# Performance work log

Measured on AMD Instinct MI355X. Metric: run time of the kernel, lower is better.

## Reference

```python
import jax, jax.numpy as jnp
import numpy as np

DIM = 100      # eqn.dim
NDIS = 50      # net_config['Ndis']
DT = 0.02      # net_config['dt']
LAM = 1.0      # HJB driver coefficient
HID = 110      # int_layers width
B = 8192       # batch


def setup_inputs() -> dict:
    key = jax.random.key(0)
    ks = jax.random.split(key, 6)
    dw = jax.random.normal(ks[0], (B, DIM, NDIS), jnp.float32) * np.float32(np.sqrt(DT))
    x = jax.random.normal(ks[1], (B, DIM, NDIS), jnp.float32)
    # z_net: Linear(dim+1 -> 110, no bias), ReLU, Linear(110 -> 110), ReLU, Linear(110 -> dim)
    W1 = (jax.random.normal(ks[2], (DIM + 1, HID), jnp.float32) / np.float32(np.sqrt(DIM + 1)))
    W2 = (jax.random.normal(ks[3], (HID, HID), jnp.float32) / np.float32(np.sqrt(HID)))
    W3 = (jax.random.normal(ks[4], (HID, DIM), jnp.float32) / np.float32(np.sqrt(HID)))
    y0 = jax.random.uniform(ks[5], (1,), jnp.float32)  # in_region=False scalar parameter
    return {"dw": dw, "x": x, "W1": W1, "W2": W2, "W3": W3, "y0": y0}


def reference(dw, x, W1, W2, W3, y0):
    # dw, x: [B, DIM, NDIS]
    ts = jnp.arange(NDIS, dtype=jnp.float32) * DT          # time_stamp
    xs = jnp.transpose(x, (2, 0, 1))                        # [T, B, DIM]
    dws = jnp.transpose(dw, (2, 0, 1))                      # [T, B, DIM]
    y_init = jnp.ones((dw.shape[0], 1), jnp.float32) * y0   # all_one_vec * y_0

    def step(y, inputs):
        t, xt, dwt = inputs
        # inp = hstack([t * all_one_vec, x[:, :, t]])  -> [B, DIM+1]
        inp = jnp.concatenate([jnp.ones((xt.shape[0], 1), xt.dtype) * t, xt], axis=1)
        h = jax.nn.relu(inp @ W1)
        h = jax.nn.relu(h @ W2)
        z = (h @ W3) / DIM                                   # [B, DIM]
        f = -LAM * jnp.sum(z * z, axis=1, keepdims=True)     # HJB driver f_tf
        y = y - DT * f + jnp.sum(z * dwt, axis=1, keepdims=True)
        return y, None

    y, _ = jax.lax.scan(step, y_init, (ts, xs, dws))
    return y  # [B, 1]
```

## Files before the change

kernel.cpp:

```cpp
#include <hip/hip_runtime.h>
#include <hip/hip_fp16.h>


#define DIMX 100
#define TS   50
#define TPAD 64
#define HID  110
#define K1   101
#define KA   120
#define NB   2
#define MROWS 128
#define DTCO 0.02f

typedef _Float16 f16;
typedef _Float16 f16x8 __attribute__((ext_vector_type(8)));
typedef float    f32x16 __attribute__((ext_vector_type(16)));

#define W1ROW 0
#define W3ROW 110
#define W2ROW 210
#define WROWS 338

__device__ __forceinline__ void mlp_layer(const f16* __restrict__ A,
                                          const f16* __restrict__ Wt,
                                          int m, int nh, int ln, int hi,
                                          f32x16& acc0, f32x16& acc1)
{
    const int arow = m * 32 + ln;
#pragma unroll
    for (int ks = 0; ks < 7; ++ks) {
        const f16x8 a   = *(const f16x8*)(A  + arow * KA            + ks * 16 + hi * 8);
        const f16x8 bv0 = *(const f16x8*)(Wt + (64 * nh      + ln) * KA + ks * 16 + hi * 8);
        const f16x8 bv1 = *(const f16x8*)(Wt + (64 * nh + 32 + ln) * KA + ks * 16 + hi * 8);
        acc0 = __builtin_amdgcn_mfma_f32_32x32x16_f16(a, bv0, acc0, 0, 0, 0);
        acc1 = __builtin_amdgcn_mfma_f32_32x32x16_f16(a, bv1, acc1, 0, 0, 0);
    }
}

__device__ __forceinline__ void store_h(f16* __restrict__ H, const f32x16& acc0,
                                        const f32x16& acc1, int m, int nh, int ln, int hi)
{
#pragma unroll
    for (int j = 0; j < 2; ++j) {
        const int col = 64 * nh + 32 * j + ln;
        if (col < HID) {
#pragma unroll
            for (int q = 0; q < 16; ++q) {
                const int row = 32 * m + (q & 3) + 8 * (q >> 2) + 4 * hi;
                float v = j ? acc1[q] : acc0[q];
                v = v > 0.f ? v : 0.f;
                H[row * KA + col] = (f16)v;
            }
        } else if (col < 112) {
#pragma unroll
            for (int q = 0; q < 16; ++q) {
                const int row = 32 * m + (q & 3) + 8 * (q >> 2) + 4 * hi;
                H[row * KA + col] = (f16)0.f;
            }
        }
    }
}

__launch_bounds__(512, 2)
__global__ void bsde_kernel(const float* __restrict__ dw, const float* __restrict__ x,
                            const float* __restrict__ W1, const float* __restrict__ W2,
                            const float* __restrict__ W3, const float* __restrict__ y0,
                            float* __restrict__ out)
{
    __shared__ __align__(16) f16 wlds[WROWS * KA];
    __shared__ __align__(16) f16 buf0[MROWS * KA];
    __shared__ __align__(16) f16 buf1[MROWS * KA];
    __shared__ float yacc[MROWS];

    const int tid  = threadIdx.x;
    const int lane = tid & 63;
    const int w    = tid >> 6;
    const int ln   = lane & 31;
    const int hi   = lane >> 5;
    const int m    = w >> 1;
    const int nh   = w & 1;

    for (int i = tid; i < WROWS * KA; i += 512) wlds[i] = (f16)0.f;
    __syncthreads();
    for (int e = tid; e < K1 * HID; e += 512) {
        const int k = e / HID, n = e % HID;
        wlds[(W1ROW + n) * KA + k] = (f16)W1[e];
    }
    for (int e = tid; e < HID * HID; e += 512) {
        const int k = e / HID, n = e % HID;
        wlds[(W2ROW + n) * KA + k] = (f16)W2[e];
    }
    for (int e = tid; e < HID * DIMX; e += 512) {
        const int k = e / DIMX, n = e % DIMX;
        wlds[(W3ROW + n) * KA + k] = (f16)W3[e];
    }
    for (int i = tid; i < MROWS * 11; i += 512) {
        const int r = i / 11, c = 101 + i % 11;
        buf0[r * KA + c] = (f16)0.f;
    }
    __syncthreads();

    const int   b0base = blockIdx.x * 32;
    const float yinit  = y0[0];

    for (int g = 0; g < 16; ++g) {
        const int b0 = b0base + 2 * g;

        if (tid < MROWS) yacc[tid] = 0.f;
        if (tid >= MROWS && tid < 2 * MROWS) {
            const int r = tid - MROWS, t = r & 63;
            buf0[r * KA] = (t < TS) ? (f16)(t * DTCO) : (f16)0.f;
        }
        for (int tau = tid; tau < NB * DIMX * 25; tau += 512) {
            const int p   = tau / (DIMX * 25);
            const int rem = tau - p * DIMX * 25;
            const int d   = rem / 25;
            const int c2  = rem - d * 25;
            const float2 v = *(const float2*)(x + ((size_t)(b0 + p) * DIMX + d) * TS + 2 * c2);
            const int r = p * TPAD + 2 * c2;
            buf0[r       * KA + 1 + d] = (f16)v.x;
            buf0[(r + 1) * KA + 1 + d] = (f16)v.y;
        }
        __syncthreads();

        {
            f32x16 a0, a1;
#pragma unroll
            for (int i = 0; i < 16; ++i) { a0[i] = 0.f; a1[i] = 0.f; }
            mlp_layer(buf0, wlds + W1ROW * KA, m, nh, ln, hi, a0, a1);
            store_h(buf1, a0, a1, m, nh, ln, hi);
        }
        __syncthreads();

        {
            f32x16 a0, a1;
#pragma unroll
            for (int i = 0; i < 16; ++i) { a0[i] = 0.f; a1[i] = 0.f; }
            mlp_layer(buf1, wlds + W2ROW * KA, m, nh, ln, hi, a0, a1);
            store_h(buf0, a0, a1, m, nh, ln, hi);
        }
        __syncthreads();

        {
            f32x16 a0, a1;
#pragma unroll
            for (int i = 0; i < 16; ++i) { a0[i] = 0.f; a1[i] = 0.f; }
            mlp_layer(buf0, wlds + W3ROW * KA, m, nh, ln, hi, a0, a1);

            float psum[16];
#pragma unroll
            for (int i = 0; i < 16; ++i) psum[i] = 0.f;

#pragma unroll
            for (int j = 0; j < 2; ++j) {
                const int d = 64 * nh + 32 * j + ln;
                if (d < DIMX) {
#pragma unroll
                    for (int qq = 0; qq < 4; ++qq) {
                        const int rbase = 32 * m + 8 * qq + 4 * hi;
                        const int t0 = rbase & 63;
                        const int p  = rbase >> 6;
                        float dv[4];
                        const float* dwp = dw + ((size_t)(b0 + p) * DIMX + d) * TS + t0;
                        if (t0 < TS)     { const float2 u = *(const float2*)dwp;       dv[0] = u.x; dv[1] = u.y; }
                        else             { dv[0] = 0.f; dv[1] = 0.f; }
                        if (t0 + 2 < TS) { const float2 u = *(const float2*)(dwp + 2); dv[2] = u.x; dv[3] = u.y; }
                        else             { dv[2] = 0.f; dv[3] = 0.f; }
#pragma unroll
                        for (int i = 0; i < 4; ++i) {
                            if (t0 + i < TS) {
                                const float z = (j ? a1[qq * 4 + i] : a0[qq * 4 + i]) * (1.0f / DIMX);
                                psum[qq * 4 + i] += DTCO * z * z + z * dv[i];
                            }
                        }
                    }
                }
            }
#pragma unroll
            for (int s = 0; s < 16; ++s) {
                float v = psum[s];
#pragma unroll
                for (int off = 1; off < 32; off <<= 1) v += __shfl_xor(v, off);
                psum[s] = v;
            }
            if (ln < 16) {
                float myv = 0.f;
#pragma unroll
                for (int s = 0; s < 16; ++s) if (ln == s) myv = psum[s];
                const int row = 32 * m + (ln & 3) + 8 * (ln >> 2) + 4 * hi;
                if ((row & 63) < TS) atomicAdd(&yacc[row], myv);
            }
        }
        __syncthreads();

        if (w < NB) {
            float v = (lane < TS) ? yacc[w * TPAD + lane] : 0.f;
#pragma unroll
            for (int off = 1; off < 64; off <<= 1) v += __shfl_xor(v, off);
            if (lane == 0) out[b0 + w] = yinit + v;
        }
        __syncthreads();
    }
}

extern "C" void kernel_launch(void* const* d_in, const int* in_sizes, int n_in,
                              void* d_out, int out_size, void* d_ws, size_t ws_size,
                              hipStream_t stream) {
    const float* dw = (const float*)d_in[0];
    const float* x  = (const float*)d_in[1];
    const float* W1 = (const float*)d_in[2];
    const float* W2 = (const float*)d_in[3];
    const float* W3 = (const float*)d_in[4];
    const float* y0 = (const float*)d_in[5];
    float* out = (float*)d_out;
    bsde_kernel<<<dim3(256), dim3(512), 0, stream>>>(dw, x, W1, W2, W3, y0, out);
}
```

Before: 466.0 us.

## Give each wave independent 32-row tiles with swizzled LDS and no block barriers

New measurement: 693.4 us. 1.49x slower.

```diff
diff --git a/kernel.cpp b/kernel.cpp
--- a/kernel.cpp
+++ b/kernel.cpp
@@ -4,202 +4,206 @@
 
 #define DIMX 100
 #define TS   50
-#define TPAD 64
 #define HID  110
-#define K1   101
-#define KA   120
-#define NB   2
-#define MROWS 128
+#define KA   128
+#define W1R  0
+#define W2R  110
+#define W3R  220
+#define WROWS 320
+#define NROWS (8192 * TS)
+#define NTILES (NROWS / 32)
+#define NWAVES 2048
 #define DTCO 0.02f
 
 typedef _Float16 f16;
 typedef _Float16 f16x8 __attribute__((ext_vector_type(8)));
 typedef float    f32x16 __attribute__((ext_vector_type(16)));
 
-#define W1ROW 0
-#define W3ROW 110
-#define W2ROW 210
-#define WROWS 338
-
-__device__ __forceinline__ void mlp_layer(const f16* __restrict__ A,
-                                          const f16* __restrict__ Wt,
-                                          int m, int nh, int ln, int hi,
-                                          f32x16& acc0, f32x16& acc1)
+__device__ __forceinline__ int swz(int row, int col) {
+    return row * KA + (col ^ ((row & 7) << 3));
+}
+
+__device__ __forceinline__ void run_layer(const f16* __restrict__ wlds, int wbase, int nmax,
+                                          const f16* __restrict__ abuf,
+                                          int ln, int hi, f32x16 acc[4])
 {
-    const int arow = m * 32 + ln;
+    const int xr = (ln & 7) << 3;
+    int brow[4], bxr[4];
+#pragma unroll
+    for (int nt = 0; nt < 4; ++nt) {
+        int n = 32 * nt + ln;
+        if (n > nmax) n = nmax;
+        brow[nt] = (wbase + n) * KA;
+        bxr[nt]  = ((wbase + n) & 7) << 3;
+    }
 #pragma unroll
     for (int ks = 0; ks < 7; ++ks) {
-        const f16x8 a   = *(const f16x8*)(A  + arow * KA            + ks * 16 + hi * 8);
-        const f16x8 bv0 = *(const f16x8*)(Wt + (64 * nh      + ln) * KA + ks * 16 + hi * 8);
-        const f16x8 bv1 = *(const f16x8*)(Wt + (64 * nh + 32 + ln) * KA + ks * 16 + hi * 8);
-        acc0 = __builtin_amdgcn_mfma_f32_32x32x16_f16(a, bv0, acc0, 0, 0, 0);
-        acc1 = __builtin_amdgcn_mfma_f32_32x32x16_f16(a, bv1, acc1, 0, 0, 0);
-    }
-}
-
-__device__ __forceinline__ void store_h(f16* __restrict__ H, const f32x16& acc0,
-                                        const f32x16& acc1, int m, int nh, int ln, int hi)
+        const int k = ks * 16 + hi * 8;
+        const f16x8 a = *(const f16x8*)(abuf + ln * KA + (k ^ xr));
+#pragma unroll
+        for (int nt = 0; nt < 4; ++nt) {
+            const f16x8 bv = *(const f16x8*)(wlds + brow[nt] + (k ^ bxr[nt]));
+            acc[nt] = __builtin_amdgcn_mfma_f32_32x32x16_f16(a, bv, acc[nt], 0, 0, 0);
+        }
+    }
+}
+
+__device__ __forceinline__ void store_h(f16* __restrict__ abuf, const f32x16 acc[4],
+                                        int ln, int hi)
 {
 #pragma unroll
-    for (int j = 0; j < 2; ++j) {
-        const int col = 64 * nh + 32 * j + ln;
-        if (col < HID) {
+    for (int nt = 0; nt < 4; ++nt) {
+        const int col = 32 * nt + ln;
+        if (col < 112) {
+            const bool live = col < HID;
 #pragma unroll
             for (int q = 0; q < 16; ++q) {
-                const int row = 32 * m + (q & 3) + 8 * (q >> 2) + 4 * hi;
-                float v = j ? acc1[q] : acc0[q];
+                const int row = (q & 3) + 8 * (q >> 2) + 4 * hi;
+                float v = live ? (float)acc[nt][q] : 0.f;
                 v = v > 0.f ? v : 0.f;
-                H[row * KA + col] = (f16)v;
+                abuf[swz(row, col)] = (f16)v;
             }
-        } else if (col < 112) {
-#pragma unroll
-            for (int q = 0; q < 16; ++q) {
-                const int row = 32 * m + (q & 3) + 8 * (q >> 2) + 4 * hi;
-                H[row * KA + col] = (f16)0.f;
-            }
-        }
-    }
+        }
+    }
+}
+
+__global__ void init_out(float* __restrict__ out, const float* __restrict__ y0) {
+    const int i = blockIdx.x * blockDim.x + threadIdx.x;
+    if (i < 8192) out[i] = y0[0];
 }
 
 __launch_bounds__(512, 2)
 __global__ void bsde_kernel(const float* __restrict__ dw, const float* __restrict__ x,
                             const float* __restrict__ W1, const float* __restrict__ W2,
-                            const float* __restrict__ W3, const float* __restrict__ y0,
-                            float* __restrict__ out)
+                            const float* __restrict__ W3, float* __restrict__ out)
 {
-    __shared__ __align__(16) f16 wlds[WROWS * KA];
-    __shared__ __align__(16) f16 buf0[MROWS * KA];
-    __shared__ __align__(16) f16 buf1[MROWS * KA];
-    __shared__ float yacc[MROWS];
+    __shared__ __align__(16) f16 lds[(WROWS + 8 * 32) * KA];
 
     const int tid  = threadIdx.x;
     const int lane = tid & 63;
     const int w    = tid >> 6;
     const int ln   = lane & 31;
     const int hi   = lane >> 5;
-    const int m    = w >> 1;
-    const int nh   = w & 1;
-
-    for (int i = tid; i < WROWS * KA; i += 512) wlds[i] = (f16)0.f;
+    f16* __restrict__ mybuf = lds + (WROWS + w * 32) * KA;
+
+    {
+        int4* p = (int4*)lds;
+        const int n16 = (WROWS + 8 * 32) * KA / 8;
+        for (int i = tid; i < n16; i += 512) p[i] = int4{0, 0, 0, 0};
+    }
     __syncthreads();
-    for (int e = tid; e < K1 * HID; e += 512) {
-        const int k = e / HID, n = e % HID;
-        wlds[(W1ROW + n) * KA + k] = (f16)W1[e];
+    for (int e = tid; e < 101 * HID; e += 512) {
+        const int k = e / HID, n = e - k * HID;
+        lds[swz(W1R + n, k)] = (f16)W1[e];
     }
     for (int e = tid; e < HID * HID; e += 512) {
-        const int k = e / HID, n = e % HID;
-        wlds[(W2ROW + n) * KA + k] = (f16)W2[e];
+        const int k = e / HID, n = e - k * HID;
+        lds[swz(W2R + n, k)] = (f16)W2[e];
     }
     for (int e = tid; e < HID * DIMX; e += 512) {
-        const int k = e / DIMX, n = e % DIMX;
-        wlds[(W3ROW + n) * KA + k] = (f16)W3[e];
-    }
-    for (int i = tid; i < MROWS * 11; i += 512) {
-        const int r = i / 11, c = 101 + i % 11;
-        buf0[r * KA + c] = (f16)0.f;
+        const int k = e / DIMX, n = e - k * DIMX;
+        lds[swz(W3R + n, k)] = (f16)W3[e];
     }
     __syncthreads();
 
-    const int   b0base = blockIdx.x * 32;
-    const float yinit  = y0[0];
-
-    for (int g = 0; g < 16; ++g) {
-        const int b0 = b0base + 2 * g;
-
-        if (tid < MROWS) yacc[tid] = 0.f;
-        if (tid >= MROWS && tid < 2 * MROWS) {
-            const int r = tid - MROWS, t = r & 63;
-            buf0[r * KA] = (t < TS) ? (f16)(t * DTCO) : (f16)0.f;
-        }
-        for (int tau = tid; tau < NB * DIMX * 25; tau += 512) {
-            const int p   = tau / (DIMX * 25);
-            const int rem = tau - p * DIMX * 25;
-            const int d   = rem / 25;
-            const int c2  = rem - d * 25;
-            const float2 v = *(const float2*)(x + ((size_t)(b0 + p) * DIMX + d) * TS + 2 * c2);
-            const int r = p * TPAD + 2 * c2;
-            buf0[r       * KA + 1 + d] = (f16)v.x;
-            buf0[(r + 1) * KA + 1 + d] = (f16)v.y;
-        }
-        __syncthreads();
+    const int wid = blockIdx.x * 8 + w;
+    const int xr  = (ln & 7) << 3;
+
+    for (int tile = wid; tile < NTILES; tile += NWAVES) {
+        const int R0 = tile * 32;
 
         {
-            f32x16 a0, a1;
-#pragma unroll
-            for (int i = 0; i < 16; ++i) { a0[i] = 0.f; a1[i] = 0.f; }
-            mlp_layer(buf0, wlds + W1ROW * KA, m, nh, ln, hi, a0, a1);
-            store_h(buf1, a0, a1, m, nh, ln, hi);
-        }
-        __syncthreads();
-
-        {
-            f32x16 a0, a1;
-#pragma unroll
-            for (int i = 0; i < 16; ++i) { a0[i] = 0.f; a1[i] = 0.f; }
-            mlp_layer(buf1, wlds + W2ROW * KA, m, nh, ln, hi, a0, a1);
-            store_h(buf0, a0, a1, m, nh, ln, hi);
-        }
-        __syncthreads();
-
-        {
-            f32x16 a0, a1;
-#pragma unroll
-            for (int i = 0; i < 16; ++i) { a0[i] = 0.f; a1[i] = 0.f; }
-            mlp_layer(buf0, wlds + W3ROW * KA, m, nh, ln, hi, a0, a1);
-
-            float psum[16];
-#pragma unroll
-            for (int i = 0; i < 16; ++i) psum[i] = 0.f;
-
-#pragma unroll
-            for (int j = 0; j < 2; ++j) {
-                const int d = 64 * nh + 32 * j + ln;
-                if (d < DIMX) {
-#pragma unroll
-                    for (int qq = 0; qq < 4; ++qq) {
-                        const int rbase = 32 * m + 8 * qq + 4 * hi;
-                        const int t0 = rbase & 63;
-                        const int p  = rbase >> 6;
-                        float dv[4];
-                        const float* dwp = dw + ((size_t)(b0 + p) * DIMX + d) * TS + t0;
-                        if (t0 < TS)     { const float2 u = *(const float2*)dwp;       dv[0] = u.x; dv[1] = u.y; }
-                        else             { dv[0] = 0.f; dv[1] = 0.f; }
-                        if (t0 + 2 < TS) { const float2 u = *(const float2*)(dwp + 2); dv[2] = u.x; dv[3] = u.y; }
-                        else             { dv[2] = 0.f; dv[3] = 0.f; }
-#pragma unroll
-                        for (int i = 0; i < 4; ++i) {
-                            if (t0 + i < TS) {
-                                const float z = (j ? a1[qq * 4 + i] : a0[qq * 4 + i]) * (1.0f / DIMX);
-                                psum[qq * 4 + i] += DTCO * z * z + z * dv[i];
-                            }
-                        }
+            const int r = R0 + ln;
+            const int b = (int)((unsigned)r / 50u);
+            const int t = r - b * 50;
+            if (hi == 0) mybuf[swz(ln, 0)] = (f16)(t * DTCO);
+            const float* __restrict__ px = x + (size_t)b * 5000 + (size_t)hi * 50 + t;
+            const int rb = ln * KA;
+#pragma unroll
+            for (int i = 0; i < 50; ++i) {
+                const int d = 2 * i + hi;
+                const float v = px[(size_t)(2 * i) * 50];
+                mybuf[rb + ((1 + d) ^ xr)] = (f16)v;
+            }
+        }
+
+        f32x16 acc[4];
+
+#pragma unroll
+        for (int nt = 0; nt < 4; ++nt)
+#pragma unroll
+            for (int q = 0; q < 16; ++q) acc[nt][q] = 0.f;
+        run_layer(lds, W1R, 109, mybuf, ln, hi, acc);
+        store_h(mybuf, acc, ln, hi);
+
+#pragma unroll
+        for (int nt = 0; nt < 4; ++nt)
+#pragma unroll
+            for (int q = 0; q < 16; ++q) acc[nt][q] = 0.f;
+        run_layer(lds, W2R, 109, mybuf, ln, hi, acc);
+        store_h(mybuf, acc, ln, hi);
+
+#pragma unroll
+        for (int nt = 0; nt < 4; ++nt)
+#pragma unroll
+            for (int q = 0; q < 16; ++q) acc[nt][q] = 0.f;
+        run_layer(lds, W3R, 99, mybuf, ln, hi, acc);
+
+        int offi[4][4];
+#pragma unroll
+        for (int qq = 0; qq < 4; ++qq) {
+            const int r = R0 + 8 * qq + 4 * hi;
+            const int b = (int)((unsigned)r / 50u);
+            const int t = r - b * 50;
+            const int off0 = b * 5000 + t;
+#pragma unroll
+            for (int i = 0; i < 4; ++i)
+                offi[qq][i] = off0 + i + ((t + i >= 50) ? 4950 : 0);
+        }
+
+        float res[16];
+#pragma unroll
+        for (int s = 0; s < 16; ++s) res[s] = 0.f;
+#pragma unroll
+        for (int nt = 0; nt < 4; ++nt) {
+            const int d = 32 * nt + ln;
+            if (d < DIMX) {
+                const float* __restrict__ base = dw + (size_t)d * 50;
+#pragma unroll
+                for (int qq = 0; qq < 4; ++qq)
+#pragma unroll
+                    for (int i = 0; i < 4; ++i) {
+                        const float dv = base[offi[qq][i]];
+                        const float z  = (float)acc[nt][qq * 4 + i] * 0.01f;
+                        res[qq * 4 + i] += z * (DTCO * z + dv);
                     }
-                }
             }
-#pragma unroll
-            for (int s = 0; s < 16; ++s) {
-                float v = psum[s];
-#pragma unroll
-                for (int off = 1; off < 32; off <<= 1) v += __shfl_xor(v, off);
-                psum[s] = v;
-            }
-            if (ln < 16) {
-                float myv = 0.f;
-#pragma unroll
-                for (int s = 0; s < 16; ++s) if (ln == s) myv = psum[s];
-                const int row = 32 * m + (ln & 3) + 8 * (ln >> 2) + 4 * hi;
-                if ((row & 63) < TS) atomicAdd(&yacc[row], myv);
-            }
-        }
-        __syncthreads();
-
-        if (w < NB) {
-            float v = (lane < TS) ? yacc[w * TPAD + lane] : 0.f;
-#pragma unroll
-            for (int off = 1; off < 64; off <<= 1) v += __shfl_xor(v, off);
-            if (lane == 0) out[b0 + w] = yinit + v;
-        }
-        __syncthreads();
+        }
+#pragma unroll
+        for (int s = 0; s < 16; ++s) {
+            float v = res[s];
+            v += __shfl_xor(v, 1);  v += __shfl_xor(v, 2);  v += __shfl_xor(v, 4);
+            v += __shfl_xor(v, 8);  v += __shfl_xor(v, 16);
+            res[s] = v;
+        }
+        float val = 0.f;
+#pragma unroll
+        for (int s = 0; s < 16; ++s) if (ln == s) val = res[s];
+        if (ln >= 16) val = 0.f;
+
+        const int rowl = (ln & 3) + 8 * ((ln >> 2) & 3) + 4 * hi;
+        const int bA = (int)((unsigned)R0 / 50u);
+        const int bB = (int)((unsigned)(R0 + 31) / 50u);
+        const int bme = (int)((unsigned)(R0 + rowl) / 50u);
+        float u0 = (bme == bA) ? val : 0.f;
+        float u1 = val - u0;
+#pragma unroll
+        for (int off = 1; off < 64; off <<= 1) {
+            u0 += __shfl_xor(u0, off);
+            u1 += __shfl_xor(u1, off);
+        }
+        if (lane == 0) atomicAdd(&out[bA], u0);
+        if (lane == 1 && bB != bA) atomicAdd(&out[bB], u1);
     }
 }
 
@@ -213,5 +217,7 @@
     const float* W3 = (const float*)d_in[4];
     const float* y0 = (const float*)d_in[5];
     float* out = (float*)d_out;
-    bsde_kernel<<<dim3(256), dim3(512), 0, stream>>>(dw, x, W1, W2, W3, y0, out);
-}
+
+    init_out<<<dim3(32), dim3(256), 0, stream>>>(out, y0);
+    bsde_kernel<<<dim3(256), dim3(512), 0, stream>>>(dw, x, W1, W2, W3, out);
+}
```
